# Kernel optimization log

Hardware: AMD Instinct MI355X
Metric: run time of the kernel (lower is better)

Reference implementation:

```python
import jax, jax.numpy as jnp
import numpy as np
from jax import lax

# Module config (UOT_loss defaults): reg_m_l2=[5.0, 5.0], div='l2',
# detach_plan=True, use_uniform=False, marginal_match_dim=1.
REG_M1, REG_M2 = 5.0, 5.0
NUM_ITER = 1000      # POT mm_unbalanced default numItermax
STOP_THR = 1e-15     # POT default stopThr
EPS = 1e-16


def pairwise_sqeuclidean(x, y):
    # ot.dist default metric='sqeuclidean': M[i,j] = ||x_i - y_j||^2
    x2 = jnp.sum(x * x, axis=1)[:, None]
    y2 = jnp.sum(y * y, axis=1)[None, :]
    return jnp.maximum(x2 + y2 - 2.0 * (x @ y.T), 0.0)


def mm_unbalanced_l2(a, b, M):
    # POT ot.unbalanced.mm_unbalanced(a, b, M, [REG_M1, REG_M2], div='l2'), reg=0.
    G0 = a[:, None] * b[None, :]                       # [n, m] init plan
    K = jnp.maximum(REG_M1 * a[:, None] + REG_M2 * b[None, :] - M, 0.0)

    def cond(state):
        i, _, err = state
        return jnp.logical_and(i < NUM_ITER, err > STOP_THR)

    def body(state):
        i, G, _ = state
        Gd = (REG_M1 * jnp.sum(G, axis=1, keepdims=True)
              + REG_M2 * jnp.sum(G, axis=0, keepdims=True) + EPS)
        Gn = K * G / Gd
        err = jnp.sqrt(jnp.sum((Gn - G) ** 2))
        return i + 1, Gn, err

    _, G, _ = lax.while_loop(
        cond, body, (jnp.int32(0), G0, jnp.array(jnp.inf, G0.dtype)))
    return G


def setup_inputs() -> dict:
    key = jax.random.key(0)
    k1, k2, k3, k4 = jax.random.split(key, 4)
    n, m, d = 4096, 4096, 64
    source = jax.random.normal(k1, (n, d), jnp.float32)
    target = jax.random.normal(k2, (m, d), jnp.float32)
    mu = jax.random.uniform(k3, (n,), jnp.float32, minval=0.5, maxval=1.5)
    nu = jax.random.uniform(k4, (m,), jnp.float32, minval=0.5, maxval=1.5)
    mu = mu / jnp.sum(mu)
    nu = nu / jnp.sum(nu)
    return {"source": source, "target": target,
            "source_density": mu, "target_density": nu}


def reference(source, target, source_density, target_density):
    M = pairwise_sqeuclidean(source, target)           # [n, m]
    plan = mm_unbalanced_l2(source_density, target_density, M)
    ot_loss = jnp.sum(plan * M)
    # marginal_match_dim=1 -> row sums (transported source mass)
    marginal_transported = jnp.sum(plan, axis=1)
    marginal_loss = jnp.mean((marginal_transported - source_density) ** 2)
    return ot_loss, marginal_loss
```

## Files before the change

### kernel.cpp

```cpp
#include <hip/hip_runtime.h>


#define NV 4096
#define RM 5.0f
#define EPSF 1e-16f
#define STOP2 1e-30f
#define NITER 1000
#define MAGIC 0x5a17c0de
#define GRID_T 512
#define NT 16384

#define ERRT_OFF 0
#define ERRS_OFF 16384
#define OTP_OFF  32768
#define RSP_OFF  49152
#define CSP_OFF  573440
#define RS_OFF   1097728
#define CS_OFF   1101824
#define BMI_OFF  1105920
#define CTL_OFF  1122304
#define G_OFF    1126400

typedef short bf16x8 __attribute__((ext_vector_type(8)));
typedef float f32x4  __attribute__((ext_vector_type(4)));
typedef unsigned short u16;

__device__ __forceinline__ float wave_sum_all(float v) {
  #pragma unroll
  for (int off = 1; off < 64; off <<= 1) v += __shfl_xor(v, off);
  return v;
}
__device__ __forceinline__ float red32_sum(float v) {
  #pragma unroll
  for (int off = 1; off < 32; off <<= 1) v += __shfl_xor(v, off);
  return v;
}
__device__ __forceinline__ float red32_max(float v) {
  #pragma unroll
  for (int off = 1; off < 32; off <<= 1) v = fmaxf(v, __shfl_xor(v, off));
  return v;
}
__device__ __forceinline__ float red16_sum(float v) {
  v += __shfl_xor(v, 1); v += __shfl_xor(v, 2);
  v += __shfl_xor(v, 4); v += __shfl_xor(v, 8);
  return v;
}
__device__ __forceinline__ float wave_sum_dn(float v) {
  #pragma unroll
  for (int off = 32; off; off >>= 1) v += __shfl_down(v, off);
  return v;
}
__device__ __forceinline__ float dot64(const float* __restrict__ xr,
                                       const float* __restrict__ yr) {
  float d = 0.f;
  #pragma unroll 1
  for (int k = 0; k < 64; ++k) d = fmaf(xr[k], yr[k], d);
  return d;
}
__device__ __forceinline__ unsigned pack2(float x, float y) {
  return (__float_as_uint(x) >> 16) | (__float_as_uint(y) & 0xffff0000u);
}

__device__ __forceinline__ void stage32(const float* __restrict__ src,
                                        u16 (*dst)[72], float* nrm, int lane) {
  #pragma unroll
  for (int it = 0; it < 8; ++it) {
    const int flat = lane + it * 64;
    const int r = flat >> 4, c4 = flat & 15;
    const float4 v = *(const float4*)(src + (size_t)r * 64 + c4 * 4);
    float p = fmaf(v.x, v.x, fmaf(v.y, v.y, fmaf(v.z, v.z, v.w * v.w)));
    p += __shfl_xor(p, 1); p += __shfl_xor(p, 2);
    p += __shfl_xor(p, 4); p += __shfl_xor(p, 8);
    if (c4 == 0) nrm[r] = p;
    uint2 w;
    w.x = pack2(v.x, v.y);
    w.y = pack2(v.z, v.w);
    *(uint2*)&dst[r][c4 * 4] = w;
  }
}

__device__ __forceinline__ void dots32(const u16 (*As)[72], const u16 (*Bs)[72],
                                       int lane, f32x4 acc[2][2]) {
  const int lrow = lane & 15, lk8 = lane >> 4;
  #pragma unroll
  for (int i = 0; i < 2; ++i)
    #pragma unroll
    for (int j = 0; j < 2; ++j)
      acc[i][j] = (f32x4){0.f, 0.f, 0.f, 0.f};
  #pragma unroll
  for (int ks = 0; ks < 2; ++ks) {
    bf16x8 af[2], bg[2];
    #pragma unroll
    for (int f = 0; f < 2; ++f) {
      af[f] = *(const bf16x8*)&As[f * 16 + lrow][ks * 32 + lk8 * 8];
      bg[f] = *(const bf16x8*)&Bs[f * 16 + lrow][ks * 32 + lk8 * 8];
    }
    #pragma unroll
    for (int fr = 0; fr < 2; ++fr)
      #pragma unroll
      for (int fc = 0; fc < 2; ++fc)
        acc[fr][fc] = __builtin_amdgcn_mfma_f32_16x16x32_bf16(
            af[fr], bg[fc], acc[fr][fc], 0, 0, 0);
  }
}

__device__ __forceinline__ void gbar(int* ctl) {
  __threadfence();
  __syncthreads();
  if (threadIdx.x == 0) {
    while (__hip_atomic_load(&ctl[2], __ATOMIC_ACQUIRE,
                             __HIP_MEMORY_SCOPE_AGENT) != (int)MAGIC)
      __builtin_amdgcn_s_sleep(8);
    const int sense = __hip_atomic_load(&ctl[1], __ATOMIC_ACQUIRE,
                                        __HIP_MEMORY_SCOPE_AGENT);
    const int old = __hip_atomic_fetch_add(&ctl[0], 1, __ATOMIC_ACQ_REL,
                                           __HIP_MEMORY_SCOPE_AGENT);
    if (old == GRID_T - 1) {
      __hip_atomic_store(&ctl[0], 0, __ATOMIC_RELAXED, __HIP_MEMORY_SCOPE_AGENT);
      __hip_atomic_store(&ctl[1], sense ^ 1, __ATOMIC_RELEASE,
                         __HIP_MEMORY_SCOPE_AGENT);
    } else {
      while (__hip_atomic_load(&ctl[1], __ATOMIC_ACQUIRE,
                               __HIP_MEMORY_SCOPE_AGENT) == sense)
        __builtin_amdgcn_s_sleep(16);
    }
  }
  __syncthreads();
  __threadfence();
}

__global__ __launch_bounds__(256, 4) void k_main(
    const float* __restrict__ X, const float* __restrict__ Y,
    const float* __restrict__ a, const float* __restrict__ b,
    float* __restrict__ W) {
  __shared__ u16 Aw[4][32][72], Bw[4][32][72];
  __shared__ float X2w[4][32], Y2w[4][32];

  const int tid = threadIdx.x, lane = tid & 63, wv = tid >> 6;
  const int lrow = lane & 15, lk8 = lane >> 4, l32 = lane & 31;
  const int t = blockIdx.x * 4 + wv;
  const int by = t >> 7, bx = t & 127;
  const int r0 = by * 32, c0 = bx * 32;
  int* bmi = (int*)(W + BMI_OFF);
  float* Gp = W + G_OFF;

  const float av = a[r0 + l32];
  const float bv = b[c0 + l32];

  stage32(X + (size_t)r0 * 64, Aw[wv], X2w[wv], lane);
  stage32(Y + (size_t)c0 * 64, Bw[wv], Y2w[wv], lane);

  f32x4 acc[2][2];
  dots32(Aw[wv], Bw[wv], lane, acc);

  float x2r[8], y2c[2];
  #pragma unroll
  for (int fr = 0; fr < 2; ++fr)
    #pragma unroll
    for (int j = 0; j < 4; ++j)
      x2r[fr * 4 + j] = X2w[wv][fr * 16 + lk8 * 4 + j];
  #pragma unroll
  for (int fc = 0; fc < 2; ++fc)
    y2c[fc] = Y2w[wv][fc * 16 + lrow];

  const float x2lv = X2w[wv][l32], y2lv = Y2w[wv][l32];
  const float amax = red32_max(av), bmax = red32_max(bv);
  const float x2m = red32_max(x2lv), y2m = red32_max(y2lv);
  const float Cw = RM * (amax + bmax) + 0.02f * sqrtf(x2m * y2m) + 0.05f;

  float mmin = 3.4e38f;
  #pragma unroll
  for (int fr = 0; fr < 2; ++fr)
    #pragma unroll
    for (int j = 0; j < 4; ++j)
      #pragma unroll
      for (int fc = 0; fc < 2; ++fc)
        mmin = fminf(mmin,
                     fmaf(-2.f, acc[fr][fc][j], x2r[fr * 4 + j] + y2c[fc]));

  if (__ballot(mmin < Cw) == 0ull) {
    const float Ea = red32_sum(av * av);
    const float Eb = red32_sum(bv * bv);
    if (lane == 0) {
      W[ERRT_OFF + t] = Ea * Eb;
      bmi[t] = 0;
    }
    return;
  }

  float sa = 0.f, sb = 0.f;
  for (int i = lane; i < NV; i += 64) { sa += a[i]; sb += b[i]; }
  sa = wave_sum_all(sa); sb = wave_sum_all(sb);
  float bcf[2], gdc[2];
  #pragma unroll
  for (int fc = 0; fc < 2; ++fc) {
    bcf[fc] = __shfl(bv, fc * 16 + lrow);
    gdc[fc] = RM * bcf[fc] * sa;
  }
  float errp = 0.f, csum[2] = {0.f, 0.f};
  int nzl = 0;
  float rs8[8];
  #pragma unroll
  for (int fr = 0; fr < 2; ++fr)
    #pragma unroll
    for (int j = 0; j < 4; ++j) {
      const int ridx = fr * 16 + lk8 * 4 + j;
      const float ar = __shfl(av, ridx);
      const float gdr = RM * ar * sb;
      const int grow = r0 + ridx;
      float rsum = 0.f;
      #pragma unroll
      for (int fc = 0; fc < 2; ++fc) {
        float Mv = fmaf(-2.f, acc[fr][fc][j], x2r[fr * 4 + j] + y2c[fc]);
        if (Mv < Cw) {
          const float dx = dot64(X + ((size_t)grow << 6),
                                 Y + ((size_t)(c0 + fc * 16 + lrow) << 6));
          Mv = x2r[fr * 4 + j] + y2c[fc] - 2.f * dx;
        }
        Mv = fmaxf(Mv, 0.f);
        const float Kv = fmaxf(RM * (ar + bcf[fc]) - Mv, 0.f);
        const float g0 = ar * bcf[fc];
        const float g = Kv * g0 / (gdr + gdc[fc] + EPSF);
        acc[fr][fc][j] = g;
        const float dl = g - g0;
        errp += dl * dl;
        nzl |= (g != 0.f);
        rsum += g;
        csum[fc] += g;
      }
      rs8[fr * 4 + j] = red16_sum(rsum);
    }
  const int nz = (__ballot(nzl) != 0ull) ? 1 : 0;
  if (nz) {
    #pragma unroll
    for (int fr = 0; fr < 2; ++fr)
      #pragma unroll
      for (int j = 0; j < 4; ++j) {
        const int ridx = fr * 16 + lk8 * 4 + j;
        const int grow = r0 + ridx;
        #pragma unroll
        for (int fc = 0; fc < 2; ++fc)
          Gp[(size_t)grow * NV + c0 + fc * 16 + lrow] = acc[fr][fc][j];
        if (lrow == 0) W[RSP_OFF + (size_t)t * 32 + ridx] = rs8[fr * 4 + j];
      }
    #pragma unroll
    for (int fc = 0; fc < 2; ++fc) {
      float cv = csum[fc];
      cv += __shfl_xor(cv, 16); cv += __shfl_xor(cv, 32);
      if (lane < 16) W[CSP_OFF + (size_t)t * 32 + fc * 16 + lrow] = cv;
    }
  }
  errp = wave_sum_all(errp);
  if (lane == 0) {
    W[ERRT_OFF + t] = errp;
    bmi[t] = nz;
  }
}

__global__ __launch_bounds__(256, 2) void k_tail(
    const float* __restrict__ X, const float* __restrict__ Y,
    const float* __restrict__ a, const float* __restrict__ b,
    float* __restrict__ W, float* __restrict__ out) {
  __shared__ u16 Aw[4][32][72], Bw[4][32][72];
  __shared__ float X2w[4][32], Y2w[4][32];
  __shared__ float serr[4], sred[4];
  __shared__ int s_any;

  const int bid = blockIdx.x, tid = threadIdx.x;
  const int lane = tid & 63, wv = tid >> 6;
  const int lrow = lane & 15, lk8 = lane >> 4, l32 = lane & 31;
  float* Gp = W + G_OFF;
  int* bmi = (int*)(W + BMI_OFF);
  int* ctl = (int*)(W + CTL_OFF);

  if (bid == 0 && tid == 0) {
    __hip_atomic_store(&ctl[0], 0, __ATOMIC_RELAXED, __HIP_MEMORY_SCOPE_AGENT);
    __hip_atomic_store(&ctl[1], 0, __ATOMIC_RELAXED, __HIP_MEMORY_SCOPE_AGENT);
    __hip_atomic_store(&ctl[2], (int)MAGIC, __ATOMIC_RELEASE,
                       __HIP_MEMORY_SCOPE_AGENT);
  }

  const int4* bmi4 = (const int4*)bmi;
  int orv = 0;
  for (int i = tid; i < 4096; i += 256) {
    const int4 q = bmi4[i];
    orv |= q.x | q.y | q.z | q.w;
  }
  if (tid == 0) s_any = 0;
  __syncthreads();
  if (orv) s_any = 1;
  __syncthreads();

  if (!s_any) {
    if (bid == 0) {
      float s = 0.f;
      for (int i = tid; i < NV; i += 256) { const float d = a[i]; s = fmaf(d, d, s); }
      s = wave_sum_dn(s);
      if (lane == 0) serr[wv] = s;
      __syncthreads();
      if (tid == 0) {
        out[0] = 0.f;
        out[1] = (serr[0] + serr[1] + serr[2] + serr[3]) * (1.0f / (float)NV);
      }
    }
    return;
  }

  int p = 2;
  while (true) {
    {
      const int sr = tid >> 5, j32 = tid & 31;
      const int r = bid * 8 + sr;
      const int byt = r >> 5, rl = r & 31;
      float vs = 0.f;
      for (int k = j32; k < 128; k += 32) {
        const int tt2 = byt * 128 + k;
        vs += bmi[tt2] ? W[RSP_OFF + (size_t)tt2 * 32 + rl] : 0.f;
      }
      vs = red32_sum(vs);
      if (j32 == 0) W[RS_OFF + r] = vs;
      float cs = 0.f;
      for (int k = j32; k < 128; k += 32) {
        const int tt2 = k * 128 + byt;
        cs += bmi[tt2] ? W[CSP_OFF + (size_t)tt2 * 32 + rl] : 0.f;
      }
      cs = red32_sum(cs);
      if (j32 == 0) W[CS_OFF + r] = cs;
    }
    if (bid == 0) {
      float e = 0.f;
      for (int i = tid; i < NT; i += 256) e += W[ERRT_OFF + i];
      e = wave_sum_all(e);
      if (lane == 0) sred[wv] = e;
      __syncthreads();
      if (tid == 0) W[ERRS_OFF] = sred[0] + sred[1] + sred[2] + sred[3];
    }
    gbar(ctl);
    const float errv = W[ERRS_OFF];
    if (errv <= STOP2 || p > NITER) break;

    #pragma unroll 1
    for (int tt = 0; tt < 8; ++tt) {
      const int t = bid * 4 + wv + tt * 2048;
      if (!bmi[t]) { if (lane == 0) W[ERRT_OFF + t] = 0.f; continue; }
      const int by = t >> 7, bx = t & 127;
      const int r0 = by * 32, c0 = bx * 32;

      const float av = a[r0 + l32], bv = b[c0 + l32];
      const float Rv = W[RS_OFF + r0 + l32], Cv = W[CS_OFF + c0 + l32];

      stage32(X + (size_t)r0 * 64, Aw[wv], X2w[wv], lane);
      stage32(Y + (size_t)c0 * 64, Bw[wv], Y2w[wv], lane);
      f32x4 acc[2][2];
      dots32(Aw[wv], Bw[wv], lane, acc);

      float x2r[8], y2c[2], bcf[2], Ccf[2];
      #pragma unroll
      for (int fr = 0; fr < 2; ++fr)
        #pragma unroll
        for (int j = 0; j < 4; ++j)
          x2r[fr * 4 + j] = X2w[wv][fr * 16 + lk8 * 4 + j];
      #pragma unroll
      for (int fc = 0; fc < 2; ++fc) {
        y2c[fc] = Y2w[wv][fc * 16 + lrow];
        bcf[fc] = __shfl(bv, fc * 16 + lrow);
        Ccf[fc] = __shfl(Cv, fc * 16 + lrow);
      }
      const float x2lv = X2w[wv][l32], y2lv = Y2w[wv][l32];
      const float amax = red32_max(av), bmax = red32_max(bv);
      const float x2m = red32_max(x2lv), y2m = red32_max(y2lv);
      const float Cw = RM * (amax + bmax) + 0.02f * sqrtf(x2m * y2m) + 0.05f;

      float errp = 0.f, csum[2] = {0.f, 0.f};
      int nzl = 0;
      float rs8[8];
      #pragma unroll
      for (int fr = 0; fr < 2; ++fr)
        #pragma unroll
        for (int j = 0; j < 4; ++j) {
          const int ridx = fr * 16 + lk8 * 4 + j;
          const float ar = __shfl(av, ridx);
          const float Rr = __shfl(Rv, ridx);
          const int grow = r0 + ridx;
          float rsum = 0.f;
          #pragma unroll
          for (int fc = 0; fc < 2; ++fc) {
            const int gcol = c0 + fc * 16 + lrow;
            const float g = Gp[(size_t)grow * NV + gcol];
            float Mv = fmaf(-2.f, acc[fr][fc][j], x2r[fr * 4 + j] + y2c[fc]);
            if (Mv < Cw) {
              const float dx = dot64(X + ((size_t)grow << 6),
                                     Y + ((size_t)gcol << 6));
              Mv = x2r[fr * 4 + j] + y2c[fc] - 2.f * dx;
            }
            Mv = fmaxf(Mv, 0.f);
            const float Kv = fmaxf(RM * (ar + bcf[fc]) - Mv, 0.f);
            const float gd = RM * Rr + RM * Ccf[fc] + EPSF;
            const float gn = Kv * g / gd;
            acc[fr][fc][j] = gn;
            const float dl = gn - g;
            errp += dl * dl;
            nzl |= (gn != 0.f);
            rsum += gn;
            csum[fc] += gn;
          }
          rs8[fr * 4 + j] = red16_sum(rsum);
        }
      const int nz = (__ballot(nzl) != 0ull) ? 1 : 0;
      #pragma unroll
      for (int fr = 0; fr < 2; ++fr)
        #pragma unroll
        for (int j = 0; j < 4; ++j) {
          const int ridx = fr * 16 + lk8 * 4 + j;
          const int grow = r0 + ridx;
          #pragma unroll
          for (int fc = 0; fc < 2; ++fc)
            Gp[(size_t)grow * NV + c0 + fc * 16 + lrow] = acc[fr][fc][j];
          if (lrow == 0) W[RSP_OFF + (size_t)t * 32 + ridx] = rs8[fr * 4 + j];
        }
      #pragma unroll
      for (int fc = 0; fc < 2; ++fc) {
        float cv = csum[fc];
        cv += __shfl_xor(cv, 16); cv += __shfl_xor(cv, 32);
        if (lane < 16) W[CSP_OFF + (size_t)t * 32 + fc * 16 + lrow] = cv;
      }
      errp = wave_sum_all(errp);
      if (lane == 0) {
        W[ERRT_OFF + t] = errp;
        bmi[t] = nz;
      }
    }
    gbar(ctl);
    ++p;
  }

  #pragma unroll 1
  for (int tt = 0; tt < 8; ++tt) {
    const int t = bid * 4 + wv + tt * 2048;
    float otw = 0.f;
    if (bmi[t]) {
      const int by = t >> 7, bx = t & 127;
      const int r0 = by * 32, c0 = bx * 32;
      float otp = 0.f;
      #pragma unroll
      for (int fr = 0; fr < 2; ++fr)
        #pragma unroll
        for (int j = 0; j < 4; ++j) {
          const int grow = r0 + fr * 16 + lk8 * 4 + j;
          #pragma unroll
          for (int fc = 0; fc < 2; ++fc) {
            const int gcol = c0 + fc * 16 + lrow;
            const float g = Gp[(size_t)grow * NV + gcol];
            if (g != 0.f) {
              const float* xr = X + ((size_t)grow << 6);
              const float* yr = Y + ((size_t)gcol << 6);
              const float dd = dot64(xr, yr);
              const float x2 = dot64(xr, xr);
              const float y2 = dot64(yr, yr);
              otp += g * fmaxf(x2 + y2 - 2.f * dd, 0.f);
            }
          }
        }
      otw = wave_sum_all(otp);
    }
    if (lane == 0) W[OTP_OFF + t] = otw;
  }
  gbar(ctl);
  if (bid == 0) {
    float so = 0.f;
    for (int i = tid; i < NT; i += 256) so += W[OTP_OFF + i];
    so = wave_sum_dn(so);
    float sm = 0.f;
    for (int i = tid; i < NV; i += 256) {
      const float d = W[RS_OFF + i] - a[i];
      sm = fmaf(d, d, sm);
    }
    sm = wave_sum_dn(sm);
    if (lane == 0) { sred[wv] = so; serr[wv] = sm; }
    __syncthreads();
    if (tid == 0) {
      out[0] = sred[0] + sred[1] + sred[2] + sred[3];
      out[1] = (serr[0] + serr[1] + serr[2] + serr[3]) * (1.0f / (float)NV);
    }
  }
}

extern "C" void kernel_launch(void* const* d_in, const int* in_sizes, int n_in,
                              void* d_out, int out_size, void* d_ws, size_t ws_size,
                              hipStream_t stream) {
  const float* X = (const float*)d_in[0];
  const float* Y = (const float*)d_in[1];
  const float* a = (const float*)d_in[2];
  const float* b = (const float*)d_in[3];
  float* out = (float*)d_out;
  float* W = (float*)d_ws;

  k_main<<<NT / 4, 256, 0, stream>>>(X, Y, a, b, W);
  k_tail<<<GRID_T, 256, 0, stream>>>(X, Y, a, b, W, out);
}
```

Before: 97.55 us.

## Replace full MFMA cost screen with Cauchy-Schwarz sub-block bound screening

Removes the per-tile MFMA pass that formed every 32x32 block of M to find blocks where K can be nonzero. A profile kernel now computes per-row norms of 16 four-element chunks, and a screen kernel uses sums of chunk-norm products as an upper bound on x·y to flag suspicious tiles with atomics. Only flagged tiles get their first iteration computed in the tail kernel, which adds a grid barrier. This is cheaper than a bf16 GEMM over all pairs, but the looser bound may flag more tiles, and the change adds two launches plus atomic traffic.

```diff
diff --git a/kernel.cpp b/kernel.cpp
--- a/kernel.cpp
+++ b/kernel.cpp
@@ -9,17 +9,27 @@
 #define MAGIC 0x5a17c0de
 #define GRID_T 512
 #define NT 16384
-
-#define ERRT_OFF 0
-#define ERRS_OFF 16384
-#define OTP_OFF  32768
-#define RSP_OFF  49152
-#define CSP_OFF  573440
-#define RS_OFF   1097728
-#define CS_OFF   1101824
-#define BMI_OFF  1105920
-#define CTL_OFF  1122304
-#define G_OFF    1126400
+#define MARGIN 1e-2f
+
+#define UP_OFF   0
+#define VP_OFF   65536
+#define X2_OFF   131072
+#define Y2_OFF   135168
+#define RA2_OFF  139264
+#define CB2_OFF  139392
+#define PA_OFF   139520
+#define PB_OFF   139648
+#define ERRT_OFF 147456
+#define ERRS_OFF 163840
+#define OTP_OFF  180224
+#define RSP_OFF  196608
+#define CSP_OFF  720896
+#define RS_OFF   1245184
+#define CS_OFF   1249280
+#define BMI_OFF  1253376
+#define SUS_OFF  1269760
+#define NSUS_OFF 1286144
+#define G_OFF    1310720
 
 typedef short bf16x8 __attribute__((ext_vector_type(8)));
 typedef float f32x4  __attribute__((ext_vector_type(4)));
@@ -38,11 +48,6 @@
 __device__ __forceinline__ float red32_max(float v) {
   #pragma unroll
   for (int off = 1; off < 32; off <<= 1) v = fmaxf(v, __shfl_xor(v, off));
-  return v;
-}
-__device__ __forceinline__ float red16_sum(float v) {
-  v += __shfl_xor(v, 1); v += __shfl_xor(v, 2);
-  v += __shfl_xor(v, 4); v += __shfl_xor(v, 8);
   return v;
 }
 __device__ __forceinline__ float wave_sum_dn(float v) {
@@ -59,6 +64,112 @@
 }
 __device__ __forceinline__ unsigned pack2(float x, float y) {
   return (__float_as_uint(x) >> 16) | (__float_as_uint(y) & 0xffff0000u);
+}
+
+__global__ __launch_bounds__(256) void k_prof(
+    const float* __restrict__ X, const float* __restrict__ Y,
+    const float* __restrict__ a, const float* __restrict__ bden,
+    float* __restrict__ W) {
+  const int bid = blockIdx.x, tid = threadIdx.x;
+  const int lane = tid & 63, wvq = tid >> 6;
+  const int lr = lane >> 3, l8 = lane & 7;
+  const int R = bid * 32 + wvq * 8 + lr;
+  const bool isX = (R < NV);
+  const int row = isX ? R : R - NV;
+  const float* src = (isX ? X : Y) + (size_t)row * 64;
+  float* UPo = W + (isX ? UP_OFF : VP_OFF) + (size_t)row * 16;
+
+  const float4 v0 = *(const float4*)(src + l8 * 8);
+  const float4 v1 = *(const float4*)(src + l8 * 8 + 4);
+  const float s0 = fmaf(v0.x, v0.x, fmaf(v0.y, v0.y, fmaf(v0.z, v0.z, v0.w * v0.w)));
+  const float s1 = fmaf(v1.x, v1.x, fmaf(v1.y, v1.y, fmaf(v1.z, v1.z, v1.w * v1.w)));
+  float2 uq; uq.x = sqrtf(s0); uq.y = sqrtf(s1);
+  *(float2*)(UPo + l8 * 2) = uq;
+  float st = s0 + s1;
+  st += __shfl_xor(st, 1); st += __shfl_xor(st, 2); st += __shfl_xor(st, 4);
+  if (l8 == 0) W[(isX ? X2_OFF : Y2_OFF) + row] = st;
+
+  if (wvq == 0 && lane < 32) {
+    if (bid < 128) {
+      const float av = a[bid * 32 + lane];
+      const float r2 = red32_sum(av * av);
+      const float pa = red32_sum(av);
+      if (lane == 0) { W[RA2_OFF + bid] = r2; W[PA_OFF + bid] = pa; }
+    } else {
+      const float bv = bden[(bid - 128) * 32 + lane];
+      const float c2 = red32_sum(bv * bv);
+      const float pb = red32_sum(bv);
+      if (lane == 0) { W[CB2_OFF + (bid - 128)] = c2; W[PB_OFF + (bid - 128)] = pb; }
+    }
+  }
+  if (tid < 64) ((int*)(W + SUS_OFF))[bid * 64 + tid] = 0;
+  if (bid == 0 && tid == 64) ((int*)(W + NSUS_OFF))[0] = 0;
+}
+
+__global__ __launch_bounds__(256, 2) void k_screen(
+    const float* __restrict__ a, const float* __restrict__ bden,
+    float* __restrict__ W) {
+  const int tid = threadIdx.x, lane = tid & 63, wv = tid >> 6;
+  const int rbase = blockIdx.x * 8;
+  const int cbase = wv * 1024;
+  const float* UP = W + UP_OFF;
+  const float* VP = W + VP_OFF;
+  int* sus  = (int*)(W + SUS_OFF);
+  int* nsus = (int*)(W + NSUS_OFF);
+
+  float u[8][16], ga[8];
+  #pragma unroll
+  for (int r = 0; r < 8; ++r) {
+    const int row = rbase + r;
+    #pragma unroll
+    for (int q = 0; q < 4; ++q) {
+      const float4 f = *(const float4*)(UP + (size_t)row * 16 + q * 4);
+      u[r][q*4+0] = f.x; u[r][q*4+1] = f.y; u[r][q*4+2] = f.z; u[r][q*4+3] = f.w;
+    }
+    ga[r] = W[X2_OFF + row] - RM * a[row] - MARGIN;
+  }
+
+  #pragma unroll 1
+  for (int k = 0; k < 8; ++k) {
+    const int col0 = cbase + lane * 2 + k * 128;
+    const float* vp = VP + (size_t)col0 * 16;
+    float v0[16], v1[16];
+    #pragma unroll
+    for (int q = 0; q < 4; ++q) {
+      const float4 f0 = *(const float4*)(vp + q * 4);
+      const float4 f1 = *(const float4*)(vp + 16 + q * 4);
+      v0[q*4+0] = f0.x; v0[q*4+1] = f0.y; v0[q*4+2] = f0.z; v0[q*4+3] = f0.w;
+      v1[q*4+0] = f1.x; v1[q*4+1] = f1.y; v1[q*4+2] = f1.z; v1[q*4+3] = f1.w;
+    }
+    const float d0 = W[Y2_OFF + col0]     - RM * bden[col0];
+    const float d1 = W[Y2_OFF + col0 + 1] - RM * bden[col0 + 1];
+
+    unsigned smask = 0u;
+    #pragma unroll
+    for (int r = 0; r < 8; ++r) {
+      float s0 = 0.f, s1 = 0.f;
+      #pragma unroll
+      for (int g = 0; g < 16; ++g) {
+        s0 = fmaf(u[r][g], v0[g], s0);
+        s1 = fmaf(u[r][g], v1[g], s1);
+      }
+      smask |= (2.f * s0 > ga[r] + d0) ? (1u << r) : 0u;
+      smask |= (2.f * s1 > ga[r] + d1) ? (1u << (r + 8)) : 0u;
+    }
+    if (__builtin_expect(smask != 0u, 0)) {
+      #pragma unroll 1
+      for (int r = 0; r < 8; ++r) {
+        if (smask & (1u << r)) {
+          atomicOr(&sus[((rbase + r) >> 5) * 128 + (col0 >> 5)], 1);
+          atomicAdd(nsus, 1);
+        }
+        if (smask & (1u << (r + 8))) {
+          atomicOr(&sus[((rbase + r) >> 5) * 128 + ((col0 + 1) >> 5)], 1);
+          atomicAdd(nsus, 1);
+        }
+      }
+    }
+  }
 }
 
 __device__ __forceinline__ void stage32(const float* __restrict__ src,
@@ -78,7 +189,6 @@
     *(uint2*)&dst[r][c4 * 4] = w;
   }
 }
-
 __device__ __forceinline__ void dots32(const u16 (*As)[72], const u16 (*Bs)[72],
                                        int lane, f32x4 acc[2][2]) {
   const int lrow = lane & 15, lk8 = lane >> 4;
@@ -103,24 +213,23 @@
             af[fr], bg[fc], acc[fr][fc], 0, 0, 0);
   }
 }
-
 __device__ __forceinline__ void gbar(int* ctl) {
   __threadfence();
   __syncthreads();
   if (threadIdx.x == 0) {
-    while (__hip_atomic_load(&ctl[2], __ATOMIC_ACQUIRE,
+    while (__hip_atomic_load(&ctl[3], __ATOMIC_ACQUIRE,
                              __HIP_MEMORY_SCOPE_AGENT) != (int)MAGIC)
       __builtin_amdgcn_s_sleep(8);
-    const int sense = __hip_atomic_load(&ctl[1], __ATOMIC_ACQUIRE,
+    const int sense = __hip_atomic_load(&ctl[2], __ATOMIC_ACQUIRE,
                                         __HIP_MEMORY_SCOPE_AGENT);
-    const int old = __hip_atomic_fetch_add(&ctl[0], 1, __ATOMIC_ACQ_REL,
+    const int old = __hip_atomic_fetch_add(&ctl[1], 1, __ATOMIC_ACQ_REL,
                                            __HIP_MEMORY_SCOPE_AGENT);
     if (old == GRID_T - 1) {
-      __hip_atomic_store(&ctl[0], 0, __ATOMIC_RELAXED, __HIP_MEMORY_SCOPE_AGENT);
-      __hip_atomic_store(&ctl[1], sense ^ 1, __ATOMIC_RELEASE,
+      __hip_atomic_store(&ctl[1], 0, __ATOMIC_RELAXED, __HIP_MEMORY_SCOPE_AGENT);
+      __hip_atomic_store(&ctl[2], sense ^ 1, __ATOMIC_RELEASE,
                          __HIP_MEMORY_SCOPE_AGENT);
     } else {
-      while (__hip_atomic_load(&ctl[1], __ATOMIC_ACQUIRE,
+      while (__hip_atomic_load(&ctl[2], __ATOMIC_ACQUIRE,
                                __HIP_MEMORY_SCOPE_AGENT) == sense)
         __builtin_amdgcn_s_sleep(16);
     }
@@ -129,169 +238,23 @@
   __threadfence();
 }
 
-__global__ __launch_bounds__(256, 4) void k_main(
-    const float* __restrict__ X, const float* __restrict__ Y,
-    const float* __restrict__ a, const float* __restrict__ b,
-    float* __restrict__ W) {
-  __shared__ u16 Aw[4][32][72], Bw[4][32][72];
-  __shared__ float X2w[4][32], Y2w[4][32];
-
-  const int tid = threadIdx.x, lane = tid & 63, wv = tid >> 6;
-  const int lrow = lane & 15, lk8 = lane >> 4, l32 = lane & 31;
-  const int t = blockIdx.x * 4 + wv;
-  const int by = t >> 7, bx = t & 127;
-  const int r0 = by * 32, c0 = bx * 32;
-  int* bmi = (int*)(W + BMI_OFF);
-  float* Gp = W + G_OFF;
-
-  const float av = a[r0 + l32];
-  const float bv = b[c0 + l32];
-
-  stage32(X + (size_t)r0 * 64, Aw[wv], X2w[wv], lane);
-  stage32(Y + (size_t)c0 * 64, Bw[wv], Y2w[wv], lane);
-
-  f32x4 acc[2][2];
-  dots32(Aw[wv], Bw[wv], lane, acc);
-
-  float x2r[8], y2c[2];
-  #pragma unroll
-  for (int fr = 0; fr < 2; ++fr)
-    #pragma unroll
-    for (int j = 0; j < 4; ++j)
-      x2r[fr * 4 + j] = X2w[wv][fr * 16 + lk8 * 4 + j];
-  #pragma unroll
-  for (int fc = 0; fc < 2; ++fc)
-    y2c[fc] = Y2w[wv][fc * 16 + lrow];
-
-  const float x2lv = X2w[wv][l32], y2lv = Y2w[wv][l32];
-  const float amax = red32_max(av), bmax = red32_max(bv);
-  const float x2m = red32_max(x2lv), y2m = red32_max(y2lv);
-  const float Cw = RM * (amax + bmax) + 0.02f * sqrtf(x2m * y2m) + 0.05f;
-
-  float mmin = 3.4e38f;
-  #pragma unroll
-  for (int fr = 0; fr < 2; ++fr)
-    #pragma unroll
-    for (int j = 0; j < 4; ++j)
-      #pragma unroll
-      for (int fc = 0; fc < 2; ++fc)
-        mmin = fminf(mmin,
-                     fmaf(-2.f, acc[fr][fc][j], x2r[fr * 4 + j] + y2c[fc]));
-
-  if (__ballot(mmin < Cw) == 0ull) {
-    const float Ea = red32_sum(av * av);
-    const float Eb = red32_sum(bv * bv);
-    if (lane == 0) {
-      W[ERRT_OFF + t] = Ea * Eb;
-      bmi[t] = 0;
-    }
-    return;
-  }
-
-  float sa = 0.f, sb = 0.f;
-  for (int i = lane; i < NV; i += 64) { sa += a[i]; sb += b[i]; }
-  sa = wave_sum_all(sa); sb = wave_sum_all(sb);
-  float bcf[2], gdc[2];
-  #pragma unroll
-  for (int fc = 0; fc < 2; ++fc) {
-    bcf[fc] = __shfl(bv, fc * 16 + lrow);
-    gdc[fc] = RM * bcf[fc] * sa;
-  }
-  float errp = 0.f, csum[2] = {0.f, 0.f};
-  int nzl = 0;
-  float rs8[8];
-  #pragma unroll
-  for (int fr = 0; fr < 2; ++fr)
-    #pragma unroll
-    for (int j = 0; j < 4; ++j) {
-      const int ridx = fr * 16 + lk8 * 4 + j;
-      const float ar = __shfl(av, ridx);
-      const float gdr = RM * ar * sb;
-      const int grow = r0 + ridx;
-      float rsum = 0.f;
-      #pragma unroll
-      for (int fc = 0; fc < 2; ++fc) {
-        float Mv = fmaf(-2.f, acc[fr][fc][j], x2r[fr * 4 + j] + y2c[fc]);
-        if (Mv < Cw) {
-          const float dx = dot64(X + ((size_t)grow << 6),
-                                 Y + ((size_t)(c0 + fc * 16 + lrow) << 6));
-          Mv = x2r[fr * 4 + j] + y2c[fc] - 2.f * dx;
-        }
-        Mv = fmaxf(Mv, 0.f);
-        const float Kv = fmaxf(RM * (ar + bcf[fc]) - Mv, 0.f);
-        const float g0 = ar * bcf[fc];
-        const float g = Kv * g0 / (gdr + gdc[fc] + EPSF);
-        acc[fr][fc][j] = g;
-        const float dl = g - g0;
-        errp += dl * dl;
-        nzl |= (g != 0.f);
-        rsum += g;
-        csum[fc] += g;
-      }
-      rs8[fr * 4 + j] = red16_sum(rsum);
-    }
-  const int nz = (__ballot(nzl) != 0ull) ? 1 : 0;
-  if (nz) {
-    #pragma unroll
-    for (int fr = 0; fr < 2; ++fr)
-      #pragma unroll
-      for (int j = 0; j < 4; ++j) {
-        const int ridx = fr * 16 + lk8 * 4 + j;
-        const int grow = r0 + ridx;
-        #pragma unroll
-        for (int fc = 0; fc < 2; ++fc)
-          Gp[(size_t)grow * NV + c0 + fc * 16 + lrow] = acc[fr][fc][j];
-        if (lrow == 0) W[RSP_OFF + (size_t)t * 32 + ridx] = rs8[fr * 4 + j];
-      }
-    #pragma unroll
-    for (int fc = 0; fc < 2; ++fc) {
-      float cv = csum[fc];
-      cv += __shfl_xor(cv, 16); cv += __shfl_xor(cv, 32);
-      if (lane < 16) W[CSP_OFF + (size_t)t * 32 + fc * 16 + lrow] = cv;
-    }
-  }
-  errp = wave_sum_all(errp);
-  if (lane == 0) {
-    W[ERRT_OFF + t] = errp;
-    bmi[t] = nz;
-  }
-}
-
 __global__ __launch_bounds__(256, 2) void k_tail(
     const float* __restrict__ X, const float* __restrict__ Y,
-    const float* __restrict__ a, const float* __restrict__ b,
+    const float* __restrict__ a, const float* __restrict__ bden,
     float* __restrict__ W, float* __restrict__ out) {
   __shared__ u16 Aw[4][32][72], Bw[4][32][72];
   __shared__ float X2w[4][32], Y2w[4][32];
   __shared__ float serr[4], sred[4];
-  __shared__ int s_any;
 
   const int bid = blockIdx.x, tid = threadIdx.x;
   const int lane = tid & 63, wv = tid >> 6;
   const int lrow = lane & 15, lk8 = lane >> 4, l32 = lane & 31;
   float* Gp = W + G_OFF;
-  int* bmi = (int*)(W + BMI_OFF);
-  int* ctl = (int*)(W + CTL_OFF);
-
-  if (bid == 0 && tid == 0) {
-    __hip_atomic_store(&ctl[0], 0, __ATOMIC_RELAXED, __HIP_MEMORY_SCOPE_AGENT);
-    __hip_atomic_store(&ctl[1], 0, __ATOMIC_RELAXED, __HIP_MEMORY_SCOPE_AGENT);
-    __hip_atomic_store(&ctl[2], (int)MAGIC, __ATOMIC_RELEASE,
-                       __HIP_MEMORY_SCOPE_AGENT);
-  }
-
-  const int4* bmi4 = (const int4*)bmi;
-  int orv = 0;
-  for (int i = tid; i < 4096; i += 256) {
-    const int4 q = bmi4[i];
-    orv |= q.x | q.y | q.z | q.w;
-  }
-  if (tid == 0) s_any = 0;
-  __syncthreads();
-  if (orv) s_any = 1;
-  __syncthreads();
-
-  if (!s_any) {
+  int* bmi  = (int*)(W + BMI_OFF);
+  int* sus  = (int*)(W + SUS_OFF);
+  int* ctl  = (int*)(W + NSUS_OFF);
+
+  if (ctl[0] == 0) {
     if (bid == 0) {
       float s = 0.f;
       for (int i = tid; i < NV; i += 256) { const float d = a[i]; s = fmaf(d, d, s); }
@@ -305,6 +268,62 @@
     }
     return;
   }
+
+  if (bid == 0 && tid == 0) {
+    __hip_atomic_store(&ctl[1], 0, __ATOMIC_RELAXED, __HIP_MEMORY_SCOPE_AGENT);
+    __hip_atomic_store(&ctl[2], 0, __ATOMIC_RELAXED, __HIP_MEMORY_SCOPE_AGENT);
+    __hip_atomic_store(&ctl[3], (int)MAGIC, __ATOMIC_RELEASE,
+                       __HIP_MEMORY_SCOPE_AGENT);
+  }
+
+  #pragma unroll 1
+  for (int tt = 0; tt < 8; ++tt) {
+    const int t = bid * 4 + wv + tt * 2048;
+    const int by = t >> 7, bx = t & 127;
+    if (!sus[t]) {
+      if (lane == 0) {
+        W[ERRT_OFF + t] = W[RA2_OFF + by] * W[CB2_OFF + bx];
+        bmi[t] = 0;
+      }
+      continue;
+    }
+    const int r0 = by * 32, c0 = bx * 32;
+    const int cl = lane & 31, h = lane >> 5;
+    float sa = W[PA_OFF + lane] + W[PA_OFF + lane + 64];
+    sa = wave_sum_all(sa);
+    float sb = W[PB_OFF + lane] + W[PB_OFF + lane + 64];
+    sb = wave_sum_all(sb);
+    const float bcl = bden[c0 + cl];
+    const float y2c = W[Y2_OFF + c0 + cl];
+    const float* yr = Y + (size_t)(c0 + cl) * 64;
+    float csum = 0.f, errp = 0.f;
+    int nzl = 0;
+    #pragma unroll 1
+    for (int r = 0; r < 16; ++r) {
+      const int row = r0 + h * 16 + r;
+      const float ar = a[row];
+      const float x2r = W[X2_OFF + row];
+      const float dx = dot64(X + (size_t)row * 64, yr);
+      const float Mv = fmaxf(x2r + y2c - 2.f * dx, 0.f);
+      const float Kv = fmaxf(RM * (ar + bcl) - Mv, 0.f);
+      const float g0 = ar * bcl;
+      const float gd = RM * ar * sb + RM * bcl * sa + EPSF;
+      const float g = Kv * g0 / gd;
+      Gp[(size_t)row * NV + c0 + cl] = g;
+      const float dl = g - g0;
+      errp += dl * dl;
+      nzl |= (g != 0.f);
+      csum += g;
+      float rsv = red32_sum(g);
+      if (cl == 0) W[RSP_OFF + (size_t)t * 32 + h * 16 + r] = rsv;
+    }
+    csum += __shfl_xor(csum, 32);
+    if (h == 0) W[CSP_OFF + (size_t)t * 32 + cl] = csum;
+    errp = wave_sum_all(errp);
+    const int nz = (__ballot(nzl) != 0ull) ? 1 : 0;
+    if (lane == 0) { W[ERRT_OFF + t] = errp; bmi[t] = nz; }
+  }
+  gbar(ctl);
 
   int p = 2;
   while (true) {
@@ -346,7 +365,7 @@
       const int by = t >> 7, bx = t & 127;
       const int r0 = by * 32, c0 = bx * 32;
 
-      const float av = a[r0 + l32], bv = b[c0 + l32];
+      const float av = a[r0 + l32], bv = bden[c0 + l32];
       const float Rv = W[RS_OFF + r0 + l32], Cv = W[CS_OFF + c0 + l32];
 
       stage32(X + (size_t)r0 * 64, Aw[wv], X2w[wv], lane);
@@ -404,7 +423,10 @@
             rsum += gn;
             csum[fc] += gn;
           }
-          rs8[fr * 4 + j] = red16_sum(rsum);
+          float rv = rsum;
+          rv += __shfl_xor(rv, 1); rv += __shfl_xor(rv, 2);
+          rv += __shfl_xor(rv, 4); rv += __shfl_xor(rv, 8);
+          rs8[fr * 4 + j] = rv;
         }
       const int nz = (__ballot(nzl) != 0ull) ? 1 : 0;
       #pragma unroll
@@ -453,10 +475,10 @@
             const float g = Gp[(size_t)grow * NV + gcol];
             if (g != 0.f) {
               const float* xr = X + ((size_t)grow << 6);
-              const float* yr = Y + ((size_t)gcol << 6);
-              const float dd = dot64(xr, yr);
+              const float* yr2 = Y + ((size_t)gcol << 6);
+              const float dd = dot64(xr, yr2);
               const float x2 = dot64(xr, xr);
-              const float y2 = dot64(yr, yr);
+              const float y2 = dot64(yr2, yr2);
               otp += g * fmaxf(x2 + y2 - 2.f * dd, 0.f);
             }
           }
@@ -495,6 +517,7 @@
   float* out = (float*)d_out;
   float* W = (float*)d_ws;
 
-  k_main<<<NT / 4, 256, 0, stream>>>(X, Y, a, b, W);
+  k_prof<<<256, 256, 0, stream>>>(X, Y, a, b, W);
+  k_screen<<<512, 256, 0, stream>>>(a, b, W);
   k_tail<<<GRID_T, 256, 0, stream>>>(X, Y, a, b, W, out);
 }
```

Measured after the change: 92.98 us. 4.7% less time.
